# Optimization experiments

Hardware: AMD Instinct MI355X
Metric: run time of the kernel (lower is better)

The kernel has to match this reference:

```python
import jax, jax.numpy as jnp
import numpy as np

WIN = (7, 7)
HW = WIN[0] * WIN[1]          # 49
C = 128
NUM_HEAD = 4
HEAD_DIM = C // NUM_HEAD
SCALE = HEAD_DIM ** -0.5
BS = 16384
NUM_WIN = 1024


def _relative_position_index():
    coords = np.stack(np.meshgrid(np.arange(WIN[0]), np.arange(WIN[1]), indexing='ij'))
    coords = coords.reshape(2, -1)                      # (2, hw)
    rel = coords[:, :, None] - coords[:, None, :]       # (2, hw, hw)
    rel = rel.transpose(1, 2, 0).copy()                 # (hw, hw, 2)
    rel[:, :, 0] += WIN[0] - 1
    rel[:, :, 1] += WIN[1] - 1
    rel[:, :, 0] *= 2 * WIN[1] - 1
    return rel.sum(-1).astype(np.int32)                 # (hw, hw)


def setup_inputs() -> dict:
    key = jax.random.key(0)
    ks = jax.random.split(key, 7)
    x = jax.random.normal(ks[0], (BS, HW, C), dtype=jnp.float32)
    mask = jax.random.normal(ks[1], (NUM_WIN, HW, HW), dtype=jnp.float32)
    qkv_w = jax.random.normal(ks[2], (3 * C, C), dtype=jnp.float32) * (C ** -0.5)
    qkv_b = jnp.zeros((3 * C,), dtype=jnp.float32)
    proj_w = jax.random.normal(ks[3], (C, C), dtype=jnp.float32) * (C ** -0.5)
    proj_b = jnp.zeros((C,), dtype=jnp.float32)
    num_rel = (2 * WIN[0] - 1) * (2 * WIN[1] - 1)       # 169
    bias_table = jax.random.normal(ks[4], (num_rel, NUM_HEAD), dtype=jnp.float32) * 0.02
    rel_index = jnp.asarray(_relative_position_index())
    return {"x": x, "mask": mask, "qkv_w": qkv_w, "qkv_b": qkv_b,
            "proj_w": proj_w, "proj_b": proj_b, "bias_table": bias_table,
            "rel_index": rel_index}


def reference(x, mask, qkv_w, qkv_b, proj_w, proj_b, bias_table, rel_index):
    bs, hw, c = x.shape
    qkv = x @ qkv_w.T + qkv_b                                   # (bs, hw, 3C)
    qkv = qkv.reshape(bs, hw, 3, NUM_HEAD, HEAD_DIM)
    qkv = jnp.transpose(qkv, (2, 0, 3, 1, 4))                   # (3, bs, H, hw, hd)
    q, k, v = qkv[0] * SCALE, qkv[1], qkv[2]
    attn = jnp.einsum('bhqd,bhkd->bhqk', q, k)                  # (bs, H, hw, hw)
    # gathered relative position bias: (hw, hw, H) -> (H, hw, hw)
    rel_bias = bias_table[rel_index.reshape(-1)].reshape(hw, hw, NUM_HEAD)
    attn = attn + jnp.transpose(rel_bias, (2, 0, 1))[None]
    nW = mask.shape[0]
    attn = attn.reshape(bs // nW, nW, NUM_HEAD, hw, hw) + mask[None, :, None]
    attn = attn.reshape(bs, NUM_HEAD, hw, hw)
    attn = jax.nn.softmax(attn, axis=-1)
    out = jnp.einsum('bhqk,bhkd->bhqd', attn, v)                # (bs, H, hw, hd)
    out = jnp.transpose(out, (0, 2, 1, 3)).reshape(bs, hw, c)
    return out @ proj_w.T + proj_b
```

## Files before the change

### kernel.cpp

```cpp
#include <hip/hip_runtime.h>
#include <hip/hip_bf16.h>

#define THREADS 512
#define WPB 8
#define NWIN 16384
#define NBLK (NWIN / WPB)

typedef short bf16x8 __attribute__((ext_vector_type(8)));
typedef float f32x4 __attribute__((ext_vector_type(4)));

#define XAP 136
#define QKP 264
#define VTP 72
#define PSP 40
#define MSP 68

#define XA_OFF 0
#define QK_OFF 6664
#define VT_OFF 19600
#define PS_OFF 28816
#define MS_OFF 33936
#define POOL_USHORTS 40600

#define LOG2E 1.4426950408889634f
#define SCALE_Q 0.17677669529663689f

#define WQ_USHORTS (96 * 64 * 8)
#define WP_USHORTS (32 * 64 * 8)

static __device__ __forceinline__ unsigned short f2bf(float x) {
    union { __hip_bfloat16 b; unsigned short u; } c;
    c.b = __float2bfloat16(x);
    return c.u;
}
static __device__ __forceinline__ unsigned pack2bf(float lo, float hi) {
    return (unsigned)f2bf(lo) | ((unsigned)f2bf(hi) << 16);
}
static __device__ __forceinline__ ushort4 cvt4(float4 v) {
    ushort4 u; u.x = f2bf(v.x); u.y = f2bf(v.y); u.z = f2bf(v.z); u.w = f2bf(v.w);
    return u;
}

__global__ __launch_bounds__(512)
void prep_weights(const float* __restrict__ qkv_w, const float* __restrict__ proj_w,
                  unsigned short* __restrict__ wq, unsigned short* __restrict__ wp)
{
    const int t = blockIdx.x * 512 + threadIdx.x;
    if (t < 96 * 64) {
        const int lane = t & 63, g = t >> 6;
        const int l16 = lane & 15, lg = lane >> 4;
        const int ks = g & 3, wn = g >> 2;
        const int ch = wn * 16 + l16;
        const float s = (ch < 128) ? (SCALE_Q * LOG2E) : 1.0f;
        const float* p = qkv_w + (size_t)ch * 128 + ks * 32 + lg * 8;
        bf16x8 f;
#pragma unroll
        for (int j = 0; j < 8; ++j) f[j] = (short)f2bf(p[j] * s);
        *(bf16x8*)&wq[(size_t)t * 8] = f;
    } else if (t < 96 * 64 + 32 * 64) {
        const int t2 = t - 96 * 64;
        const int lane = t2 & 63, g = t2 >> 6;
        const int l16 = lane & 15, lg = lane >> 4;
        const int ks = g & 3, wv = g >> 2;
        const float* p = proj_w + (size_t)(wv * 16 + l16) * 128 + ks * 32 + lg * 8;
        bf16x8 f;
#pragma unroll
        for (int j = 0; j < 8; ++j) f[j] = (short)f2bf(p[j]);
        *(bf16x8*)&wp[(size_t)t2 * 8] = f;
    }
}

__global__ __launch_bounds__(THREADS, 4)
void winattn_kernel(const float* __restrict__ x, const float* __restrict__ mask,
                    const unsigned short* __restrict__ wq, const unsigned short* __restrict__ wpr,
                    const float* __restrict__ qkv_b, const float* __restrict__ proj_b,
                    const float* __restrict__ bias_table, const int* __restrict__ rel_index,
                    float* __restrict__ out)
{
    __shared__ __align__(16) unsigned short pool[POOL_USHORTS];
    float* maskF = (float*)&pool[MS_OFF];

    const int tid  = threadIdx.x;
    const int wave = tid >> 6;
    const int lane = tid & 63;
    const int lg   = lane >> 4;
    const int l16  = lane & 15;
    const int h    = wave >> 1;
    const int mh   = wave & 1;

    unsigned biasP[2][4][2];
#pragma unroll
    for (int nt = 0; nt < 2; ++nt) {
        int qt = mh * 32 + nt * 16 + l16; if (qt > 48) qt = 48;
#pragma unroll
        for (int mt = 0; mt < 4; ++mt) {
#pragma unroll
            for (int w2 = 0; w2 < 2; ++w2) {
                float b[2];
#pragma unroll
                for (int r = 0; r < 2; ++r) {
                    int kt = mt * 16 + lg * 4 + w2 * 2 + r; if (kt > 48) kt = 48;
                    const int idx = rel_index[qt * 49 + kt];
                    b[r] = bias_table[idx * 4 + h] * LOG2E;
                }
                biasP[nt][mt][w2] = pack2bf(b[0], b[1]);
            }
        }
    }
    const float4 pb = *(const float4*)(proj_b + wave * 16 + lg * 4);

    const int win0 = blockIdx.x * WPB;

    {
        unsigned* p32 = (unsigned*)pool;
        for (int i = QK_OFF / 2 + tid; i < QK_OFF / 2 + (12936 + 9216) / 2; i += THREADS)
            p32[i] = 0;
    }
#pragma unroll
    for (int it = 0; it < 4; ++it) {
        const int e = it * 2048 + tid * 4;
        if (e < 6272) {
            float4 v = *(const float4*)(x + (size_t)win0 * 6272 + e);
            *(ushort4*)&pool[XA_OFF + (e >> 7) * XAP + (e & 127)] = cvt4(v);
        }
    }
    {
        const float* mp0 = mask + (size_t)(win0 & 1023) * 2401;
        for (int e = tid; e < 2401; e += THREADS)
            maskF[(e / 49) * MSP + (e % 49)] = mp0[e] * LOG2E;
    }
    __syncthreads();

    for (int w = 0; w < WPB; ++w) {
        const int win = win0 + w;
        const bool pf = (w + 1 < WPB);

        {
            uintptr_t wqu = (uintptr_t)wq;
            asm volatile("" : "+s"(wqu));
            const unsigned short* wqx = (const unsigned short*)wqu;
#pragma unroll
            for (int nt = 0; nt < 3; ++nt) {
                bf16x8 wB[4];
#pragma unroll
                for (int ks = 0; ks < 4; ++ks)
                    wB[ks] = *(const bf16x8*)&wqx[(size_t)(((wave * 3 + nt) * 4 + ks) * 64 + lane) * 8];
                const int chB = wave * 48 + nt * 16;
                float4 qb4;
                if (chB < 256) {
                    qb4 = *(const float4*)(qkv_b + chB + lg * 4);
                    if (chB < 128) { qb4.x *= SCALE_Q * LOG2E; qb4.y *= SCALE_Q * LOG2E;
                                     qb4.z *= SCALE_Q * LOG2E; qb4.w *= SCALE_Q * LOG2E; }
                } else {
                    qb4.x = qkv_b[chB + l16];
                }
#pragma unroll
                for (int mt = 0; mt < 4; ++mt) {
                    bf16x8 xf[4];
#pragma unroll
                    for (int ks = 0; ks < 4; ++ks)
                        xf[ks] = *(const bf16x8*)&pool[XA_OFF + (mt * 16 + l16) * XAP + ks * 32 + lg * 8];
                    f32x4 acc = (f32x4){0.f, 0.f, 0.f, 0.f};
                    if (chB < 256) {
#pragma unroll
                        for (int ks = 0; ks < 4; ++ks)
                            acc = __builtin_amdgcn_mfma_f32_16x16x32_bf16(wB[ks], xf[ks], acc, 0, 0, 0);
                        const int tok = mt * 16 + l16;
                        if (tok < 49) {
                            float4 v; v.x = acc[0] + qb4.x; v.y = acc[1] + qb4.y;
                            v.z = acc[2] + qb4.z; v.w = acc[3] + qb4.w;
                            *(ushort4*)&pool[QK_OFF + tok * QKP + chB + lg * 4] = cvt4(v);
                        }
                    } else {
#pragma unroll
                        for (int ks = 0; ks < 4; ++ks)
                            acc = __builtin_amdgcn_mfma_f32_16x16x32_bf16(xf[ks], wB[ks], acc, 0, 0, 0);
                        const float vb = qb4.x;
                        float4 v; v.x = acc[0] + vb; v.y = acc[1] + vb;
                        v.z = acc[2] + vb; v.w = acc[3] + vb;
                        *(ushort4*)&pool[VT_OFF + (chB - 256 + l16) * VTP + mt * 16 + lg * 4] = cvt4(v);
                    }
                }
            }
        }
        __syncthreads();

        bf16x8 ak[4];
#pragma unroll
        for (int mt = 0; mt < 4; ++mt)
            ak[mt] = *(const bf16x8*)&pool[QK_OFF + (mt * 16 + l16) * QKP + 128 + h * 32 + lg * 8];

        float inv[2];
        unsigned pk[2][4][2];
#pragma unroll
        for (int nt = 0; nt < 2; ++nt) {
            const bf16x8 bq = *(const bf16x8*)&pool[QK_OFF + (mh * 32 + nt * 16 + l16) * QKP + h * 32 + lg * 8];
            f32x4 S[4];
#pragma unroll
            for (int mt = 0; mt < 4; ++mt)
                S[mt] = __builtin_amdgcn_mfma_f32_16x16x32_bf16(ak[mt], bq, (f32x4){0.f,0.f,0.f,0.f}, 0, 0, 0);

            const int qt = mh * 32 + nt * 16 + l16;
            const bool qok = (qt < 49);
            const int qrow = qok ? qt : 48;
            float lv[4][4];
#pragma unroll
            for (int mt = 0; mt < 4; ++mt) {
                const float4 mm = *(const float4*)&maskF[qrow * MSP + mt * 16 + lg * 4];
                const unsigned b0 = biasP[nt][mt][0], b1 = biasP[nt][mt][1];
                const float bb0 = __uint_as_float(b0 << 16);
                const float bb1 = __uint_as_float(b0 & 0xffff0000u);
                const float bb2 = __uint_as_float(b1 << 16);
                const float bb3 = __uint_as_float(b1 & 0xffff0000u);
                const int kt0 = mt * 16 + lg * 4;
                lv[mt][0] = (qok && kt0 + 0 < 49) ? (S[mt][0] + bb0 + mm.x) : -1e30f;
                lv[mt][1] = (qok && kt0 + 1 < 49) ? (S[mt][1] + bb1 + mm.y) : -1e30f;
                lv[mt][2] = (qok && kt0 + 2 < 49) ? (S[mt][2] + bb2 + mm.z) : -1e30f;
                lv[mt][3] = (qok && kt0 + 3 < 49) ? (S[mt][3] + bb3 + mm.w) : -1e30f;
            }
            float mx = lv[0][0];
#pragma unroll
            for (int mt = 0; mt < 4; ++mt)
#pragma unroll
                for (int r = 0; r < 4; ++r) mx = fmaxf(mx, lv[mt][r]);
            mx = fmaxf(mx, __shfl_xor(mx, 16));
            mx = fmaxf(mx, __shfl_xor(mx, 32));
            float sum = 0.f;
#pragma unroll
            for (int mt = 0; mt < 4; ++mt)
#pragma unroll
                for (int r = 0; r < 4; ++r) {
                    const float p = exp2f(lv[mt][r] - mx);
                    lv[mt][r] = p;
                    sum += p;
                }
            sum += __shfl_xor(sum, 16);
            sum += __shfl_xor(sum, 32);
            inv[nt] = 1.0f / sum;
#pragma unroll
            for (int mt = 0; mt < 4; ++mt) {
                pk[nt][mt][0] = pack2bf(lv[mt][0], lv[mt][1]);
                pk[nt][mt][1] = pack2bf(lv[mt][2], lv[mt][3]);
            }
        }

        f32x4 O[2][2];
#pragma unroll
        for (int i = 0; i < 2; ++i)
#pragma unroll
            for (int j = 0; j < 2; ++j) O[i][j] = (f32x4){0.f, 0.f, 0.f, 0.f};
        const int psb = PS_OFF + wave * 16 * PSP;
#pragma unroll
        for (int kh = 0; kh < 2; ++kh) {
            bf16x8 bv[2];
#pragma unroll
            for (int i = 0; i < 2; ++i)
                bv[i] = *(const bf16x8*)&pool[VT_OFF + (h * 32 + i * 16 + l16) * VTP + kh * 32 + lg * 8];
#pragma unroll
            for (int j = 0; j < 2; ++j) {
                uint2 t0, t1;
                t0.x = pk[j][2 * kh + 0][0]; t0.y = pk[j][2 * kh + 0][1];
                t1.x = pk[j][2 * kh + 1][0]; t1.y = pk[j][2 * kh + 1][1];
                *(uint2*)&pool[psb + l16 * PSP + lg * 4]      = t0;
                *(uint2*)&pool[psb + l16 * PSP + 16 + lg * 4] = t1;
                asm volatile("s_waitcnt lgkmcnt(0)" ::: "memory");
                __builtin_amdgcn_sched_barrier(0);
                const bf16x8 pa = *(const bf16x8*)&pool[psb + l16 * PSP + lg * 8];
#pragma unroll
                for (int i = 0; i < 2; ++i)
                    O[i][j] = __builtin_amdgcn_mfma_f32_16x16x32_bf16(bv[i], pa, O[i][j], 0, 0, 0);
            }
        }
#pragma unroll
        for (int j = 0; j < 2; ++j) {
            const int tok = mh * 32 + j * 16 + l16;
            if (tok < 49) {
#pragma unroll
                for (int i = 0; i < 2; ++i) {
                    float4 v;
                    v.x = O[i][j][0] * inv[j]; v.y = O[i][j][1] * inv[j];
                    v.z = O[i][j][2] * inv[j]; v.w = O[i][j][3] * inv[j];
                    *(ushort4*)&pool[XA_OFF + tok * XAP + h * 32 + i * 16 + lg * 4] = cvt4(v);
                }
            }
        }
        __syncthreads();

        if (pf) {
            const float* mp1 = mask + (size_t)((win + 1) & 1023) * 2401;
            for (int e = tid; e < 2401; e += THREADS)
                maskF[(e / 49) * MSP + (e % 49)] = mp1[e] * LOG2E;
        }

        bf16x8 wp_[4];
        {
            uintptr_t wpu = (uintptr_t)wpr;
            asm volatile("" : "+s"(wpu));
            const unsigned short* wpx = (const unsigned short*)wpu;
#pragma unroll
            for (int ks = 0; ks < 4; ++ks)
                wp_[ks] = *(const bf16x8*)&wpx[(size_t)((wave * 4 + ks) * 64 + lane) * 8];
        }
#pragma unroll
        for (int nt4 = 0; nt4 < 4; ++nt4) {
            f32x4 pc = (f32x4){0.f, 0.f, 0.f, 0.f};
#pragma unroll
            for (int ks = 0; ks < 4; ++ks) {
                const bf16x8 bfr = *(const bf16x8*)&pool[XA_OFF + (nt4 * 16 + l16) * XAP + ks * 32 + lg * 8];
                pc = __builtin_amdgcn_mfma_f32_16x16x32_bf16(wp_[ks], bfr, pc, 0, 0, 0);
            }
            const int tok = nt4 * 16 + l16;
            if (tok < 49) {
                float4 o;
                o.x = pc[0] + pb.x; o.y = pc[1] + pb.y;
                o.z = pc[2] + pb.z; o.w = pc[3] + pb.w;
                *(float4*)(out + ((size_t)win * 49 + tok) * 128 + wave * 16 + lg * 4) = o;
            }
        }
        __syncthreads();

        if (pf) {
            const float* xp1 = x + (size_t)(win + 1) * 6272;
#pragma unroll
            for (int it = 0; it < 4; ++it) {
                const int e = it * 2048 + tid * 4;
                if (e < 6272) {
                    float4 v = *(const float4*)(xp1 + e);
                    *(ushort4*)&pool[XA_OFF + (e >> 7) * XAP + (e & 127)] = cvt4(v);
                }
            }
        }
        __syncthreads();
    }
}

extern "C" void kernel_launch(void* const* d_in, const int* in_sizes, int n_in,
                              void* d_out, int out_size, void* d_ws, size_t ws_size,
                              hipStream_t stream) {
    const float* x          = (const float*)d_in[0];
    const float* mask       = (const float*)d_in[1];
    const float* qkv_w      = (const float*)d_in[2];
    const float* qkv_b      = (const float*)d_in[3];
    const float* proj_w     = (const float*)d_in[4];
    const float* proj_b     = (const float*)d_in[5];
    const float* bias_table = (const float*)d_in[6];
    const int*   rel_index  = (const int*)d_in[7];
    float* out = (float*)d_out;
    (void)in_sizes; (void)n_in; (void)ws_size; (void)out_size;

    unsigned short* wq = (unsigned short*)d_ws;
    unsigned short* wp = wq + WQ_USHORTS;

    prep_weights<<<dim3(16), dim3(512), 0, stream>>>(qkv_w, proj_w, wq, wp);
    winattn_kernel<<<dim3(NBLK), dim3(THREADS), 0, stream>>>(
        x, mask, wq, wp, qkv_b, proj_b, bias_table, rel_index, out);
}
```

Baseline: 454.0 us.

## Precombine mask and relative bias, double-buffer x tile to overlap loads

A new prep kernel folds the window mask and the gathered relative position bias (scaled by log2e) into one padded per-window, per-head fp32 table. The attention kernel then reads these logit offsets straight from global memory instead of staging the mask in LDS and holding the bias in registers. The freed LDS holds a second x buffer, so the next window's input is loaded at the start of each iteration and one barrier is removed. Costs are an extra ~40MB table written and reread each call, extra global reads in the softmax, and hardcoded assumptions about masked key columns.

```diff
diff --git a/kernel.cpp b/kernel.cpp
--- a/kernel.cpp
+++ b/kernel.cpp
@@ -13,18 +13,19 @@
 #define QKP 264
 #define VTP 72
 #define PSP 40
-#define MSP 68
-
-#define XA_OFF 0
-#define QK_OFF 6664
-#define VT_OFF 19600
-#define PS_OFF 28816
-#define MS_OFF 33936
+
+#define XA0_OFF 0
+#define XA1_OFF 6664
+#define QK_OFF  13328
+#define VT_OFF  26264
+#define PS_OFF  35480
 #define POOL_USHORTS 40600
 
 #define LOG2E 1.4426950408889634f
 #define SCALE_Q 0.17677669529663689f
 
+#define COMB_FLOATS (1024 * 4 * 49 * 52)
+#define COMB_BYTES  ((size_t)COMB_FLOATS * 4)
 #define WQ_USHORTS (96 * 64 * 8)
 #define WP_USHORTS (32 * 64 * 8)
 
@@ -70,15 +71,30 @@
     }
 }
 
+__global__ __launch_bounds__(512)
+void prep_comb(const float* __restrict__ mask, const float* __restrict__ bias_table,
+               const int* __restrict__ rel_index, float* __restrict__ comb)
+{
+    const unsigned t = blockIdx.x * 512 + threadIdx.x;
+    if (t >= 1024u * 4u * 49u * 49u) return;
+    const unsigned wi = t / 9604u;
+    const unsigned r1 = t - wi * 9604u;
+    const unsigned h  = r1 / 2401u;
+    const unsigned r2 = r1 - h * 2401u;
+    const unsigned qt = r2 / 49u;
+    const unsigned kt = r2 - qt * 49u;
+    const float m = mask[wi * 2401u + r2];
+    const float b = bias_table[rel_index[r2] * 4 + h];
+    comb[(((size_t)wi * 4u + h) * 49u + qt) * 52u + kt] = (m + b) * LOG2E;
+}
+
 __global__ __launch_bounds__(THREADS, 4)
-void winattn_kernel(const float* __restrict__ x, const float* __restrict__ mask,
+void winattn_kernel(const float* __restrict__ x, const float* __restrict__ comb,
                     const unsigned short* __restrict__ wq, const unsigned short* __restrict__ wpr,
                     const float* __restrict__ qkv_b, const float* __restrict__ proj_b,
-                    const float* __restrict__ bias_table, const int* __restrict__ rel_index,
                     float* __restrict__ out)
 {
     __shared__ __align__(16) unsigned short pool[POOL_USHORTS];
-    float* maskF = (float*)&pool[MS_OFF];
 
     const int tid  = threadIdx.x;
     const int wave = tid >> 6;
@@ -88,32 +104,13 @@
     const int h    = wave >> 1;
     const int mh   = wave & 1;
 
-    unsigned biasP[2][4][2];
-#pragma unroll
-    for (int nt = 0; nt < 2; ++nt) {
-        int qt = mh * 32 + nt * 16 + l16; if (qt > 48) qt = 48;
-#pragma unroll
-        for (int mt = 0; mt < 4; ++mt) {
-#pragma unroll
-            for (int w2 = 0; w2 < 2; ++w2) {
-                float b[2];
-#pragma unroll
-                for (int r = 0; r < 2; ++r) {
-                    int kt = mt * 16 + lg * 4 + w2 * 2 + r; if (kt > 48) kt = 48;
-                    const int idx = rel_index[qt * 49 + kt];
-                    b[r] = bias_table[idx * 4 + h] * LOG2E;
-                }
-                biasP[nt][mt][w2] = pack2bf(b[0], b[1]);
-            }
-        }
-    }
     const float4 pb = *(const float4*)(proj_b + wave * 16 + lg * 4);
 
     const int win0 = blockIdx.x * WPB;
 
     {
         unsigned* p32 = (unsigned*)pool;
-        for (int i = QK_OFF / 2 + tid; i < QK_OFF / 2 + (12936 + 9216) / 2; i += THREADS)
+        for (int i = QK_OFF / 2 + tid; i < (QK_OFF + 12936 + 9216) / 2; i += THREADS)
             p32[i] = 0;
     }
 #pragma unroll
@@ -121,19 +118,28 @@
         const int e = it * 2048 + tid * 4;
         if (e < 6272) {
             float4 v = *(const float4*)(x + (size_t)win0 * 6272 + e);
-            *(ushort4*)&pool[XA_OFF + (e >> 7) * XAP + (e & 127)] = cvt4(v);
-        }
-    }
-    {
-        const float* mp0 = mask + (size_t)(win0 & 1023) * 2401;
-        for (int e = tid; e < 2401; e += THREADS)
-            maskF[(e / 49) * MSP + (e % 49)] = mp0[e] * LOG2E;
+            *(ushort4*)&pool[XA0_OFF + (e >> 7) * XAP + (e & 127)] = cvt4(v);
+        }
     }
     __syncthreads();
 
     for (int w = 0; w < WPB; ++w) {
         const int win = win0 + w;
         const bool pf = (w + 1 < WPB);
+        const int xaC = (w & 1) ? XA1_OFF : XA0_OFF;
+        const int xaN = (w & 1) ? XA0_OFF : XA1_OFF;
+
+        if (pf) {
+            const float* xp1 = x + (size_t)(win + 1) * 6272;
+#pragma unroll
+            for (int it = 0; it < 4; ++it) {
+                const int e = it * 2048 + tid * 4;
+                if (e < 6272) {
+                    float4 v = *(const float4*)(xp1 + e);
+                    *(ushort4*)&pool[xaN + (e >> 7) * XAP + (e & 127)] = cvt4(v);
+                }
+            }
+        }
 
         {
             uintptr_t wqu = (uintptr_t)wq;
@@ -159,7 +165,7 @@
                     bf16x8 xf[4];
 #pragma unroll
                     for (int ks = 0; ks < 4; ++ks)
-                        xf[ks] = *(const bf16x8*)&pool[XA_OFF + (mt * 16 + l16) * XAP + ks * 32 + lg * 8];
+                        xf[ks] = *(const bf16x8*)&pool[xaC + (mt * 16 + l16) * XAP + ks * 32 + lg * 8];
                     f32x4 acc = (f32x4){0.f, 0.f, 0.f, 0.f};
                     if (chB < 256) {
 #pragma unroll
@@ -185,63 +191,55 @@
         }
         __syncthreads();
 
-        bf16x8 ak[4];
-#pragma unroll
-        for (int mt = 0; mt < 4; ++mt)
-            ak[mt] = *(const bf16x8*)&pool[QK_OFF + (mt * 16 + l16) * QKP + 128 + h * 32 + lg * 8];
-
+        const float* combW = comb + ((size_t)((win & 1023) * 4 + h)) * (49 * 52);
         float inv[2];
         unsigned pk[2][4][2];
 #pragma unroll
         for (int nt = 0; nt < 2; ++nt) {
-            const bf16x8 bq = *(const bf16x8*)&pool[QK_OFF + (mh * 32 + nt * 16 + l16) * QKP + h * 32 + lg * 8];
+            const int qt = mh * 32 + nt * 16 + l16;
+            const int qrow = (qt > 48) ? 48 : qt;
+            const float* crow = combW + qrow * 52;
+            const float4 c0 = *(const float4*)(crow + lg * 4);
+            const float4 c1 = *(const float4*)(crow + 16 + lg * 4);
+            const float4 c2 = *(const float4*)(crow + 32 + lg * 4);
+            const float  c3 = crow[48];
+            const bf16x8 bq = *(const bf16x8*)&pool[QK_OFF + qt * QKP + h * 32 + lg * 8];
             f32x4 S[4];
 #pragma unroll
-            for (int mt = 0; mt < 4; ++mt)
-                S[mt] = __builtin_amdgcn_mfma_f32_16x16x32_bf16(ak[mt], bq, (f32x4){0.f,0.f,0.f,0.f}, 0, 0, 0);
-
-            const int qt = mh * 32 + nt * 16 + l16;
-            const bool qok = (qt < 49);
-            const int qrow = qok ? qt : 48;
-            float lv[4][4];
-#pragma unroll
             for (int mt = 0; mt < 4; ++mt) {
-                const float4 mm = *(const float4*)&maskF[qrow * MSP + mt * 16 + lg * 4];
-                const unsigned b0 = biasP[nt][mt][0], b1 = biasP[nt][mt][1];
-                const float bb0 = __uint_as_float(b0 << 16);
-                const float bb1 = __uint_as_float(b0 & 0xffff0000u);
-                const float bb2 = __uint_as_float(b1 << 16);
-                const float bb3 = __uint_as_float(b1 & 0xffff0000u);
-                const int kt0 = mt * 16 + lg * 4;
-                lv[mt][0] = (qok && kt0 + 0 < 49) ? (S[mt][0] + bb0 + mm.x) : -1e30f;
-                lv[mt][1] = (qok && kt0 + 1 < 49) ? (S[mt][1] + bb1 + mm.y) : -1e30f;
-                lv[mt][2] = (qok && kt0 + 2 < 49) ? (S[mt][2] + bb2 + mm.z) : -1e30f;
-                lv[mt][3] = (qok && kt0 + 3 < 49) ? (S[mt][3] + bb3 + mm.w) : -1e30f;
-            }
-            float mx = lv[0][0];
-#pragma unroll
-            for (int mt = 0; mt < 4; ++mt)
-#pragma unroll
-                for (int r = 0; r < 4; ++r) mx = fmaxf(mx, lv[mt][r]);
+                const bf16x8 ak = *(const bf16x8*)&pool[QK_OFF + (mt * 16 + l16) * QKP + 128 + h * 32 + lg * 8];
+                S[mt] = __builtin_amdgcn_mfma_f32_16x16x32_bf16(ak, bq, (f32x4){0.f,0.f,0.f,0.f}, 0, 0, 0);
+            }
+            float lv[12];
+            lv[0] = S[0][0] + c0.x; lv[1] = S[0][1] + c0.y;
+            lv[2] = S[0][2] + c0.z; lv[3] = S[0][3] + c0.w;
+            lv[4] = S[1][0] + c1.x; lv[5] = S[1][1] + c1.y;
+            lv[6] = S[1][2] + c1.z; lv[7] = S[1][3] + c1.w;
+            lv[8] = S[2][0] + c2.x; lv[9] = S[2][1] + c2.y;
+            lv[10] = S[2][2] + c2.z; lv[11] = S[2][3] + c2.w;
+            const float lv3 = (lg == 0) ? (S[3][0] + c3) : -1e30f;
+
+            float mx = lv3;
+#pragma unroll
+            for (int i = 0; i < 12; ++i) mx = fmaxf(mx, lv[i]);
             mx = fmaxf(mx, __shfl_xor(mx, 16));
             mx = fmaxf(mx, __shfl_xor(mx, 32));
             float sum = 0.f;
 #pragma unroll
-            for (int mt = 0; mt < 4; ++mt)
-#pragma unroll
-                for (int r = 0; r < 4; ++r) {
-                    const float p = exp2f(lv[mt][r] - mx);
-                    lv[mt][r] = p;
-                    sum += p;
-                }
+            for (int i = 0; i < 12; ++i) {
+                const float p = exp2f(lv[i] - mx);
+                lv[i] = p;
+                sum += p;
+            }
+            const float p3 = exp2f(lv3 - mx);
+            sum += p3;
             sum += __shfl_xor(sum, 16);
             sum += __shfl_xor(sum, 32);
             inv[nt] = 1.0f / sum;
-#pragma unroll
-            for (int mt = 0; mt < 4; ++mt) {
-                pk[nt][mt][0] = pack2bf(lv[mt][0], lv[mt][1]);
-                pk[nt][mt][1] = pack2bf(lv[mt][2], lv[mt][3]);
-            }
+            pk[nt][0][0] = pack2bf(lv[0], lv[1]);  pk[nt][0][1] = pack2bf(lv[2], lv[3]);
+            pk[nt][1][0] = pack2bf(lv[4], lv[5]);  pk[nt][1][1] = pack2bf(lv[6], lv[7]);
+            pk[nt][2][0] = pack2bf(lv[8], lv[9]);  pk[nt][2][1] = pack2bf(lv[10], lv[11]);
+            pk[nt][3][0] = pack2bf(p3, 0.f);       pk[nt][3][1] = 0u;
         }
 
         f32x4 O[2][2];
@@ -280,17 +278,11 @@
                     float4 v;
                     v.x = O[i][j][0] * inv[j]; v.y = O[i][j][1] * inv[j];
                     v.z = O[i][j][2] * inv[j]; v.w = O[i][j][3] * inv[j];
-                    *(ushort4*)&pool[XA_OFF + tok * XAP + h * 32 + i * 16 + lg * 4] = cvt4(v);
+                    *(ushort4*)&pool[xaC + tok * XAP + h * 32 + i * 16 + lg * 4] = cvt4(v);
                 }
             }
         }
         __syncthreads();
-
-        if (pf) {
-            const float* mp1 = mask + (size_t)((win + 1) & 1023) * 2401;
-            for (int e = tid; e < 2401; e += THREADS)
-                maskF[(e / 49) * MSP + (e % 49)] = mp1[e] * LOG2E;
-        }
 
         bf16x8 wp_[4];
         {
@@ -306,7 +298,7 @@
             f32x4 pc = (f32x4){0.f, 0.f, 0.f, 0.f};
 #pragma unroll
             for (int ks = 0; ks < 4; ++ks) {
-                const bf16x8 bfr = *(const bf16x8*)&pool[XA_OFF + (nt4 * 16 + l16) * XAP + ks * 32 + lg * 8];
+                const bf16x8 bfr = *(const bf16x8*)&pool[xaC + (nt4 * 16 + l16) * XAP + ks * 32 + lg * 8];
                 pc = __builtin_amdgcn_mfma_f32_16x16x32_bf16(wp_[ks], bfr, pc, 0, 0, 0);
             }
             const int tok = nt4 * 16 + l16;
@@ -315,19 +307,6 @@
                 o.x = pc[0] + pb.x; o.y = pc[1] + pb.y;
                 o.z = pc[2] + pb.z; o.w = pc[3] + pb.w;
                 *(float4*)(out + ((size_t)win * 49 + tok) * 128 + wave * 16 + lg * 4) = o;
-            }
-        }
-        __syncthreads();
-
-        if (pf) {
-            const float* xp1 = x + (size_t)(win + 1) * 6272;
-#pragma unroll
-            for (int it = 0; it < 4; ++it) {
-                const int e = it * 2048 + tid * 4;
-                if (e < 6272) {
-                    float4 v = *(const float4*)(xp1 + e);
-                    *(ushort4*)&pool[XA_OFF + (e >> 7) * XAP + (e & 127)] = cvt4(v);
-                }
             }
         }
         __syncthreads();
@@ -348,10 +327,12 @@
     float* out = (float*)d_out;
     (void)in_sizes; (void)n_in; (void)ws_size; (void)out_size;
 
-    unsigned short* wq = (unsigned short*)d_ws;
+    float* comb = (float*)d_ws;
+    unsigned short* wq = (unsigned short*)((char*)d_ws + COMB_BYTES);
     unsigned short* wp = wq + WQ_USHORTS;
 
     prep_weights<<<dim3(16), dim3(512), 0, stream>>>(qkv_w, proj_w, wq, wp);
+    prep_comb<<<dim3(19208), dim3(512), 0, stream>>>(mask, bias_table, rel_index, comb);
     winattn_kernel<<<dim3(NBLK), dim3(THREADS), 0, stream>>>(
-        x, mask, wq, wp, qkv_b, proj_b, bias_table, rel_index, out);
-}
+        x, comb, wq, wp, qkv_b, proj_b, out);
+}
```

Result: faster. 416.2 us (-8.3%).
